# Kernel tuning notes

Hardware: AMD Instinct MI355X
Metric: run time of the kernel (lower is better)

## Reference

```python
import jax, jax.numpy as jnp
import numpy as np

B, S, D, H = 2, 2048, 1024, 16
HD = D // H  # head_dim = 64


def setup_inputs() -> dict:
    key = jax.random.key(0)
    ks = jax.random.split(key, 9)
    scale = 0.02
    x = jax.random.normal(ks[0], (B, S, D), dtype=jnp.float32)
    wq = jax.random.normal(ks[1], (D, D), dtype=jnp.float32) * scale
    bq = jnp.zeros((D,), dtype=jnp.float32)
    wk = jax.random.normal(ks[2], (D, D), dtype=jnp.float32) * scale
    bk = jnp.zeros((D,), dtype=jnp.float32)
    wv = jax.random.normal(ks[3], (D, D), dtype=jnp.float32) * scale
    bv = jnp.zeros((D,), dtype=jnp.float32)
    wo = jax.random.normal(ks[4], (D, D), dtype=jnp.float32) * scale
    bo = jnp.zeros((D,), dtype=jnp.float32)
    # causal mask: 1.0 where key position is in the future of query position
    mask = jnp.triu(jnp.ones((S, S), dtype=jnp.float32), k=1)[None, None]  # [1,1,S,S]
    return {"x": x, "wq": wq, "bq": bq, "wk": wk, "bk": bk,
            "wv": wv, "bv": bv, "wo": wo, "bo": bo, "mask": mask}


def reference(x, wq, bq, wk, bk, wv, bv, wo, bo, mask):
    b, s, d = x.shape
    q = (x @ wq + bq).reshape(b, s, H, HD).transpose(0, 2, 1, 3)  # [b,h,s,hd]
    k = (x @ wk + bk).reshape(b, s, H, HD).transpose(0, 2, 1, 3)
    v = (x @ wv + bv).reshape(b, s, H, HD).transpose(0, 2, 1, 3)
    scores = jnp.einsum('bhqd,bhkd->bhqk', q, k) / jnp.sqrt(jnp.float32(HD))
    scores = scores + mask * (-1e9)
    probs = jax.nn.softmax(scores, axis=-1)
    out = jnp.einsum('bhqk,bhkd->bhqd', probs, v)
    out = out.transpose(0, 2, 1, 3).reshape(b, s, d)
    return out @ wo + bo
```

## Files before the change

kernel.cpp:

```cpp
#include <hip/hip_runtime.h>
#include <hip/hip_bf16.h>
#include <cstdint>

#define DEV static __device__ __forceinline__

typedef unsigned short u16t;
typedef __attribute__((ext_vector_type(4))) float f32x4;
typedef __attribute__((ext_vector_type(4))) unsigned short u16x4;
typedef __attribute__((ext_vector_type(8))) unsigned short u16x8;
typedef __attribute__((ext_vector_type(8))) __bf16 bf16x8;

DEV u16t f2bf(float f) {
  unsigned u = __builtin_bit_cast(unsigned, f);
  u += 0x7fffu + ((u >> 16) & 1u);
  return (u16t)(u >> 16);
}
DEV float bf2f(u16t h) {
  unsigned u = ((unsigned)h) << 16;
  return __builtin_bit_cast(float, u);
}

DEV void gload_lds16(const void* g, void* l) {
  __builtin_amdgcn_global_load_lds(
      (const __attribute__((address_space(1))) void*)g,
      (__attribute__((address_space(3))) void*)l, 16, 0, 0);
}

DEV bf16x8 ldsfrag(const u16t* p) {
  return __builtin_bit_cast(bf16x8, *(const u16x8*)p);
}

__global__ __launch_bounds__(256) void k_convert_x(const float* __restrict__ x,
                                                   u16t* __restrict__ xb) {
  int i = (blockIdx.x * 256 + threadIdx.x) * 4;
  f32x4 v = *(const f32x4*)&x[i];
  u16x4 o;
#pragma unroll
  for (int j = 0; j < 4; ++j) o[j] = f2bf(v[j]);
  *(u16x4*)&xb[i] = o;
}

__global__ __launch_bounds__(256) void k_transw(const float* __restrict__ w0,
                                                const float* __restrict__ w1,
                                                const float* __restrict__ w2,
                                                const float* __restrict__ w3,
                                                u16t* __restrict__ qkvT,
                                                u16t* __restrict__ oT) {
  __shared__ float lds[64][68];
  int z = blockIdx.z;
  const float* W = (z == 0) ? w0 : (z == 1) ? w1 : (z == 2) ? w2 : w3;
  u16t* OUT = (z < 3) ? (qkvT + (size_t)z * 1024 * 1024) : oT;
  int k0 = blockIdx.x * 64, n0 = blockIdx.y * 64;
  int t = threadIdx.x;
  int kl = t >> 4, n4 = (t & 15) << 2;
#pragma unroll
  for (int p = 0; p < 4; ++p) {
    f32x4 v = *(const f32x4*)&W[(size_t)(k0 + kl + p * 16) * 1024 + n0 + n4];
    *(f32x4*)&lds[kl + p * 16][n4] = v;
  }
  __syncthreads();
  int nl = t >> 4, k4 = (t & 15) << 2;
#pragma unroll
  for (int p = 0; p < 4; ++p) {
    int n = nl + p * 16;
    u16x4 o;
#pragma unroll
    for (int i = 0; i < 4; ++i) o[i] = f2bf(lds[k4 + i][n]);
    *(u16x4*)&OUT[(size_t)(n0 + n) * 1024 + k0 + k4] = o;
  }
}

template <bool BF16_OUT, bool VSPLIT>
__global__ __launch_bounds__(256) void k_gemm_bt(const u16t* __restrict__ A,
                                                 const u16t* __restrict__ BT,
                                                 void* __restrict__ Cout,
                                                 const float* __restrict__ b0,
                                                 const float* __restrict__ b1,
                                                 const float* __restrict__ b2,
                                                 u16t* __restrict__ vt,
                                                 int M, int N, int K) {
  __shared__ u16t Al[128 * 64];
  __shared__ u16t Bl[128 * 64];
  const int tid = threadIdx.x;
  const int l = tid & 63;
  const int w = tid >> 6;
  const int m0 = blockIdx.x * 128, n0 = blockIdx.y * 128;
  const int wm = (w >> 1) * 64, wn = (w & 1) * 64;
  const int lm = l & 15, lh = l >> 4;
  f32x4 acc[4][4] = {};

  const int nt = K >> 6;
  for (int t = 0; t < nt; ++t) {
    const int k0 = t << 6;
#pragma unroll
    for (int s = 0; s < 4; ++s) {
      int c = s * 256 + tid;
      int row = c >> 3, slot = c & 7;
      int ks = k0 + (((slot ^ (row & 7)) & 7) << 3);
      gload_lds16(A + (size_t)(m0 + row) * K + ks, &Al[c * 8]);
    }
#pragma unroll
    for (int s = 0; s < 4; ++s) {
      int c = s * 256 + tid;
      int row = c >> 3, slot = c & 7;
      int ks = k0 + (((slot ^ (row & 7)) & 7) << 3);
      gload_lds16(BT + (size_t)(n0 + row) * K + ks, &Bl[c * 8]);
    }
    asm volatile("s_waitcnt vmcnt(0)" ::: "memory");
    __syncthreads();

#pragma unroll
    for (int kk = 0; kk < 2; ++kk) {
      bf16x8 af[4], bfr[4];
#pragma unroll
      for (int i = 0; i < 4; ++i) {
        int ra = wm + i * 16 + lm;
        int sa = (kk * 4 + lh) ^ (ra & 7);
        af[i] = ldsfrag(&Al[ra * 64 + sa * 8]);
        int rb = wn + i * 16 + lm;
        int sb = (kk * 4 + lh) ^ (rb & 7);
        bfr[i] = ldsfrag(&Bl[rb * 64 + sb * 8]);
      }
#pragma unroll
      for (int i = 0; i < 4; ++i)
#pragma unroll
        for (int j = 0; j < 4; ++j)
          acc[i][j] = __builtin_amdgcn_mfma_f32_16x16x32_bf16(af[i], bfr[j],
                                                              acc[i][j], 0, 0, 0);
    }
    __syncthreads();
  }

  if (!VSPLIT || (n0 + wn) < 2048) {
#pragma unroll
    for (int i = 0; i < 4; ++i) {
      int row = m0 + wm + i * 16 + (lh << 2);
#pragma unroll
      for (int j = 0; j < 4; ++j) {
        int col = n0 + wn + j * 16 + lm;
        const float* bp = (col < 1024) ? b0 : ((col < 2048) ? b1 : b2);
        float bias = bp[col & 1023];
#pragma unroll
        for (int r = 0; r < 4; ++r) {
          float v = acc[i][j][r] + bias;
          if (BF16_OUT)
            ((u16t*)Cout)[(size_t)(row + r) * N + col] = f2bf(v);
          else
            ((float*)Cout)[(size_t)(row + r) * N + col] = v;
        }
      }
    }
  } else {
#pragma unroll
    for (int i = 0; i < 4; ++i) {
      int row = m0 + wm + i * 16 + (lh << 2);
      int bidx = row >> 11, s0 = row & 2047;
#pragma unroll
    for (int j = 0; j < 4; ++j) {
        int col = n0 + wn + j * 16 + lm;
        int d = col - 2048;
        int hh = d >> 6, dd = d & 63;
        float bias = b2[d];
        u16x4 o;
#pragma unroll
        for (int r = 0; r < 4; ++r) o[r] = f2bf(acc[i][j][r] + bias);
        *(u16x4*)&vt[((size_t)((bidx * 16 + hh) * 64 + dd)) * 2048 + s0] = o;
      }
    }
  }
}

__global__ __launch_bounds__(256, 4) void k_attn(const u16t* __restrict__ qkv,
                                                 const u16t* __restrict__ vt,
                                                 u16t* __restrict__ outp) {
  __shared__ u16t Kl[2][4096];
  __shared__ u16t Vl[2][4096];
  __shared__ u16t Pl[4][1024];
  const int tid = threadIdx.x, l = tid & 63, w = tid >> 6;
  const int lm = l & 15, lh = l >> 4;
  const int bh = blockIdx.x, b = bh >> 4, h = bh & 15;
  const int y = blockIdx.y;
  const int qt = (y < 8) ? y : (y < 16) ? (39 - y) : (y < 24) ? (y - 8) : (47 - y);
  const int q0 = qt * 64;
  const int nt = qt + 1;

  bf16x8 aq[2];
  const int qrow = q0 + w * 16 + lm;
#pragma unroll
  for (int kk = 0; kk < 2; ++kk) {
    const u16t* src = qkv + (size_t)(b * 2048 + qrow) * 3072 + h * 64 + kk * 32 + lh * 8;
    u16x8 v = *(const u16x8*)src;
    u16x8 o;
#pragma unroll
    for (int e = 0; e < 8; ++e) o[e] = f2bf(bf2f(v[e]) * 0.125f);
    aq[kk] = __builtin_bit_cast(bf16x8, o);
  }

  float mrun = -1e30f;
  float lsum = 0.f;
  f32x4 aco[4] = {};

  const u16t* Kg = qkv + (size_t)b * 2048 * 3072 + 1024 + h * 64;
  const u16t* Vg = vt + (size_t)bh * 64 * 2048;
  u16t* Pw = &Pl[w][0];

  auto stage = [&](int buf, int t) {
#pragma unroll
    for (int s = 0; s < 2; ++s) {
      int c = s * 256 + tid;
      int row = c >> 3, col = ((c & 7) ^ (row & 7)) << 3;
      gload_lds16(Kg + (size_t)(t * 64 + row) * 3072 + col, &Kl[buf][c * 8]);
    }
#pragma unroll
    for (int s = 0; s < 2; ++s) {
      int c = s * 256 + tid;
      int row = c >> 3, col = ((c & 7) ^ (row & 7)) << 3;
      gload_lds16(Vg + (size_t)row * 2048 + t * 64 + col, &Vl[buf][c * 8]);
    }
  };

  stage(0, 0);
  asm volatile("s_waitcnt vmcnt(0)" ::: "memory");
  __syncthreads();

  int buf = 0;
  for (int t = 0; t < nt; ++t) {
    if (t + 1 < nt) stage(buf ^ 1, t + 1);

    f32x4 accs[4] = {};
#pragma unroll
    for (int kk = 0; kk < 2; ++kk) {
      bf16x8 ak[4];
#pragma unroll
      for (int nk = 0; nk < 4; ++nk) {
        int rk = nk * 16 + lm;
        int s16 = (kk * 4 + lh) ^ (rk & 7);
        ak[nk] = ldsfrag(&Kl[buf][rk * 64 + s16 * 8]);
      }
      __builtin_amdgcn_s_setprio(1);
#pragma unroll
      for (int nk = 0; nk < 4; ++nk)
        accs[nk] = __builtin_amdgcn_mfma_f32_16x16x32_bf16(ak[nk], aq[kk],
                                                           accs[nk], 0, 0, 0);
      __builtin_amdgcn_s_setprio(0);
    }

    float vmax = -1e30f;
#pragma unroll
    for (int nk = 0; nk < 4; ++nk)
#pragma unroll
      for (int r = 0; r < 4; ++r) {
        int kvpos = t * 64 + nk * 16 + lh * 4 + r;
        float v = accs[nk][r];
        v = (kvpos > qrow) ? -1e30f : v;
        accs[nk][r] = v;
        vmax = fmaxf(vmax, v);
      }

    if (!__all(vmax <= mrun + 8.f)) {
      float rm = fmaxf(vmax, __shfl_xor(vmax, 16));
      rm = fmaxf(rm, __shfl_xor(rm, 32));
      float mnew = fmaxf(mrun, rm);
      float alpha = __expf(mrun - mnew);
      mrun = mnew;
      lsum *= alpha;
#pragma unroll
      for (int r = 0; r < 4; ++r) {
        float ar = __shfl(alpha, lh * 4 + r);
#pragma unroll
        for (int nd = 0; nd < 4; ++nd) aco[nd][r] *= ar;
      }
    }

#pragma unroll
    for (int nk = 0; nk < 4; ++nk) {
      u16x4 pb;
#pragma unroll
      for (int r = 0; r < 4; ++r) {
        float p = __expf(accs[nk][r] - mrun);
        lsum += p;
        pb[r] = f2bf(p);
      }
      int s16 = (nk * 2 + (lh >> 1)) ^ (lm & 7);
      *(u16x4*)&Pw[lm * 64 + s16 * 8 + (lh & 1) * 4] = pb;
    }

#pragma unroll
    for (int kk = 0; kk < 2; ++kk) {
      int s16p = (kk * 4 + lh) ^ (lm & 7);
      bf16x8 ap = ldsfrag(&Pw[lm * 64 + s16p * 8]);
      __builtin_amdgcn_s_setprio(1);
#pragma unroll
      for (int nd = 0; nd < 4; ++nd) {
        int rv = nd * 16 + lm;
        int s16v = (kk * 4 + lh) ^ (rv & 7);
        bf16x8 bv = ldsfrag(&Vl[buf][rv * 64 + s16v * 8]);
        aco[nd] = __builtin_amdgcn_mfma_f32_16x16x32_bf16(ap, bv, aco[nd], 0, 0, 0);
      }
      __builtin_amdgcn_s_setprio(0);
    }

    asm volatile("s_waitcnt vmcnt(0)" ::: "memory");
    __syncthreads();
    buf ^= 1;
  }

  lsum += __shfl_xor(lsum, 16);
  lsum += __shfl_xor(lsum, 32);
  float inv = 1.0f / lsum;
#pragma unroll
  for (int r = 0; r < 4; ++r) {
    float ir = __shfl(inv, lh * 4 + r);
    int row = q0 + w * 16 + lh * 4 + r;
#pragma unroll
    for (int nd = 0; nd < 4; ++nd) {
      int col = h * 64 + nd * 16 + lm;
      outp[(size_t)(b * 2048 + row) * 1024 + col] = f2bf(aco[nd][r] * ir);
    }
  }
}

extern "C" void kernel_launch(void* const* d_in, const int* in_sizes, int n_in,
                              void* d_out, int out_size, void* d_ws, size_t ws_size,
                              hipStream_t stream) {
  const float* x = (const float*)d_in[0];
  const float* wq = (const float*)d_in[1];
  const float* bq = (const float*)d_in[2];
  const float* wk = (const float*)d_in[3];
  const float* bk = (const float*)d_in[4];
  const float* wv = (const float*)d_in[5];
  const float* bv = (const float*)d_in[6];
  const float* wo = (const float*)d_in[7];
  const float* bo = (const float*)d_in[8];

  char* ws = (char*)d_ws;
  u16t* xb = (u16t*)ws;
  u16t* wqkvT = (u16t*)(ws + (8u << 20));
  u16t* woT = (u16t*)(ws + (14u << 20));
  u16t* qkv = (u16t*)(ws + (16u << 20));
  u16t* vt = (u16t*)(ws + (40u << 20));
  u16t* attn_out = xb;

  k_convert_x<<<4096, 256, 0, stream>>>(x, xb);
  k_transw<<<dim3(16, 16, 4), 256, 0, stream>>>(wq, wk, wv, wo, wqkvT, woT);
  k_gemm_bt<true, true><<<dim3(32, 24), 256, 0, stream>>>(xb, wqkvT, qkv, bq, bk,
                                                          bv, vt, 4096, 3072, 1024);
  k_attn<<<dim3(32, 32), 256, 0, stream>>>(qkv, vt, attn_out);
  k_gemm_bt<false, false><<<dim3(32, 8), 256, 0, stream>>>(
      attn_out, woT, d_out, bo, bo, bo, nullptr, 4096, 1024, 1024);
}
```

Before: 121.4 us.

## Double-buffer GEMM LDS tiles and defer attention waits to next-iteration barrier

The projection GEMM now uses two LDS buffers, so the loads for the next K tile are issued before computing the current one, with a partial vmcnt wait in place of a full drain. The attention loop likewise moves its wait to the top of the next iteration with a partial count, letting prefetch overlap compute. The causal mask is applied only on the diagonal tile, skipping compares elsewhere. The GEMM doubles its LDS footprint, which may reduce occupancy, and correctness depends on the hand-counted vmcnt values matching the number of issued loads.

After: 112.7 us. 7.2% less time.

```diff
diff --git a/kernel.cpp b/kernel.cpp
--- a/kernel.cpp
+++ b/kernel.cpp
@@ -28,6 +28,12 @@
 
 DEV bf16x8 ldsfrag(const u16t* p) {
   return __builtin_bit_cast(bf16x8, *(const u16x8*)p);
+}
+
+DEV void bsync() {
+  asm volatile("" ::: "memory");
+  __builtin_amdgcn_s_barrier();
+  asm volatile("" ::: "memory");
 }
 
 __global__ __launch_bounds__(256) void k_convert_x(const float* __restrict__ x,
@@ -79,8 +85,8 @@
                                                  const float* __restrict__ b2,
                                                  u16t* __restrict__ vt,
                                                  int M, int N, int K) {
-  __shared__ u16t Al[128 * 64];
-  __shared__ u16t Bl[128 * 64];
+  __shared__ u16t Al[2][128 * 64];
+  __shared__ u16t Bl[2][128 * 64];
   const int tid = threadIdx.x;
   const int l = tid & 63;
   const int w = tid >> 6;
@@ -89,25 +95,35 @@
   const int lm = l & 15, lh = l >> 4;
   f32x4 acc[4][4] = {};
 
-  const int nt = K >> 6;
-  for (int t = 0; t < nt; ++t) {
+  auto stage = [&](int bb, int t) {
     const int k0 = t << 6;
 #pragma unroll
     for (int s = 0; s < 4; ++s) {
       int c = s * 256 + tid;
       int row = c >> 3, slot = c & 7;
       int ks = k0 + (((slot ^ (row & 7)) & 7) << 3);
-      gload_lds16(A + (size_t)(m0 + row) * K + ks, &Al[c * 8]);
+      gload_lds16(A + (size_t)(m0 + row) * K + ks, &Al[bb][c * 8]);
     }
 #pragma unroll
     for (int s = 0; s < 4; ++s) {
       int c = s * 256 + tid;
       int row = c >> 3, slot = c & 7;
       int ks = k0 + (((slot ^ (row & 7)) & 7) << 3);
-      gload_lds16(BT + (size_t)(n0 + row) * K + ks, &Bl[c * 8]);
-    }
-    asm volatile("s_waitcnt vmcnt(0)" ::: "memory");
-    __syncthreads();
+      gload_lds16(BT + (size_t)(n0 + row) * K + ks, &Bl[bb][c * 8]);
+    }
+  };
+
+  const int nt = K >> 6;
+  stage(0, 0);
+  for (int t = 0; t < nt; ++t) {
+    if (t + 1 < nt) {
+      stage((t + 1) & 1, t + 1);
+      asm volatile("s_waitcnt vmcnt(8)" ::: "memory");
+    } else {
+      asm volatile("s_waitcnt vmcnt(0)" ::: "memory");
+    }
+    bsync();
+    const int buf = t & 1;
 
 #pragma unroll
     for (int kk = 0; kk < 2; ++kk) {
@@ -116,10 +132,10 @@
       for (int i = 0; i < 4; ++i) {
         int ra = wm + i * 16 + lm;
         int sa = (kk * 4 + lh) ^ (ra & 7);
-        af[i] = ldsfrag(&Al[ra * 64 + sa * 8]);
+        af[i] = ldsfrag(&Al[buf][ra * 64 + sa * 8]);
         int rb = wn + i * 16 + lm;
         int sb = (kk * 4 + lh) ^ (rb & 7);
-        bfr[i] = ldsfrag(&Bl[rb * 64 + sb * 8]);
+        bfr[i] = ldsfrag(&Bl[buf][rb * 64 + sb * 8]);
       }
 #pragma unroll
       for (int i = 0; i < 4; ++i)
@@ -128,7 +144,7 @@
           acc[i][j] = __builtin_amdgcn_mfma_f32_16x16x32_bf16(af[i], bfr[j],
                                                               acc[i][j], 0, 0, 0);
     }
-    __syncthreads();
+    bsync();
   }
 
   if (!VSPLIT || (n0 + wn) < 2048) {
@@ -220,12 +236,16 @@
   };
 
   stage(0, 0);
-  asm volatile("s_waitcnt vmcnt(0)" ::: "memory");
-  __syncthreads();
 
   int buf = 0;
   for (int t = 0; t < nt; ++t) {
-    if (t + 1 < nt) stage(buf ^ 1, t + 1);
+    if (t + 1 < nt) {
+      stage(buf ^ 1, t + 1);
+      asm volatile("s_waitcnt vmcnt(4)" ::: "memory");
+    } else {
+      asm volatile("s_waitcnt vmcnt(0)" ::: "memory");
+    }
+    bsync();
 
     f32x4 accs[4] = {};
 #pragma unroll
@@ -246,16 +266,23 @@
     }
 
     float vmax = -1e30f;
-#pragma unroll
-    for (int nk = 0; nk < 4; ++nk)
-#pragma unroll
-      for (int r = 0; r < 4; ++r) {
-        int kvpos = t * 64 + nk * 16 + lh * 4 + r;
-        float v = accs[nk][r];
-        v = (kvpos > qrow) ? -1e30f : v;
-        accs[nk][r] = v;
-        vmax = fmaxf(vmax, v);
-      }
+    if (t == nt - 1) {
+#pragma unroll
+      for (int nk = 0; nk < 4; ++nk)
+#pragma unroll
+        for (int r = 0; r < 4; ++r) {
+          int kvpos = t * 64 + nk * 16 + lh * 4 + r;
+          float v = accs[nk][r];
+          v = (kvpos > qrow) ? -1e30f : v;
+          accs[nk][r] = v;
+          vmax = fmaxf(vmax, v);
+        }
+    } else {
+#pragma unroll
+      for (int nk = 0; nk < 4; ++nk)
+#pragma unroll
+        for (int r = 0; r < 4; ++r) vmax = fmaxf(vmax, accs[nk][r]);
+    }
 
     if (!__all(vmax <= mrun + 8.f)) {
       float rm = fmaxf(vmax, __shfl_xor(vmax, 16));
@@ -300,8 +327,7 @@
       __builtin_amdgcn_s_setprio(0);
     }
 
-    asm volatile("s_waitcnt vmcnt(0)" ::: "memory");
-    __syncthreads();
+    bsync();
     buf ^= 1;
   }
 
```
